# Kernel optimization log

Hardware: AMD Instinct MI355X
Metric: run time of the kernel (lower is better)

The kernel has to match this reference:

```python
import jax, jax.numpy as jnp
import numpy as np

N, NS, D, HID = 8192, 512, 1024, 1024  # nodes, num_edges, f_dim, mlp hidden (max(f_dim,128))


def layernorm(x, g, b, eps=1e-5):
    m = x.mean(-1, keepdims=True)
    v = x.var(-1, keepdims=True)
    return (x - m) / jnp.sqrt(v + eps) * g + b


def mask_topk(a, kk):
    # keep only the top-kk entries of each row (vectorized version of mask_attn)
    _, idx = jax.lax.top_k(a, kk)
    rows = jnp.arange(a.shape[0])[:, None]
    mask = jnp.zeros(a.shape, a.dtype).at[rows, idx].set(1.0)
    return a * mask


def setup_inputs() -> dict:
    key = jax.random.key(0)
    ks = jax.random.split(key, 16)
    xavier = lambda k, i, o: jax.random.uniform(k, (i, o), jnp.float32, -1.0, 1.0) * np.sqrt(6.0 / (i + o))
    return {
        "inputs": jax.random.normal(ks[0], (N, D), jnp.float32),
        "noise": jax.random.normal(ks[1], (NS, D), jnp.float32),
        "edges_mu": jax.random.normal(ks[2], (1, D), jnp.float32),
        "edges_logsigma": xavier(ks[3], 1, D),
        "Wq": xavier(ks[4], D, D), "bq": jnp.zeros((D,), jnp.float32),
        "Wk": xavier(ks[5], D, D), "bk": jnp.zeros((D,), jnp.float32),
        "Wv": xavier(ks[6], D, D), "bv": jnp.zeros((D,), jnp.float32),
        "W1": xavier(ks[7], 2 * D, HID), "b1": jnp.zeros((HID,), jnp.float32),
        "W2": xavier(ks[8], HID, D), "b2": jnp.zeros((D,), jnp.float32),
        "g_in": jnp.ones((D,), jnp.float32), "b_in": jnp.zeros((D,), jnp.float32),
        "g_e": jnp.ones((D,), jnp.float32), "b_e": jnp.zeros((D,), jnp.float32),
        "k_n": 64,
        "k_e": 8,
    }


def reference(inputs, noise, edges_mu, edges_logsigma, Wq, bq, Wk, bk, Wv, bv,
              W1, b1, W2, b2, g_in, b_in, g_e, b_e, k_n, k_e):
    n, d = inputs.shape
    scale = d ** -0.5
    eps = 1e-8
    x = layernorm(inputs, g_in, b_in)                       # norm_input
    k = jax.nn.relu(x @ Wk + bk)                            # [N, D]
    v = jax.nn.relu(x @ Wv + bv)                            # [N, D]
    edges = edges_mu + jnp.exp(edges_logsigma) * noise      # [NS, D]
    # single iteration (iters=1)
    edges = layernorm(edges, g_e, b_e)                      # norm_edgs
    q = jax.nn.relu(edges @ Wq + bq)                        # [NS, D]
    dots = jnp.einsum('ni,mi->nm', q, k) * scale            # [NS, N]
    attn = jax.nn.softmax(dots, axis=1) + eps
    attn = attn / attn.sum(axis=1, keepdims=True)
    attn = mask_topk(attn, k_n)
    updates = jnp.einsum('nm,md->nd', attn, v)              # [NS, D]
    edges = jnp.concatenate([edges, updates], axis=1)       # [NS, 2D]
    edges = jax.nn.relu(edges @ W1 + b1) @ W2 + b2          # mlp -> [NS, D]
    q2 = x @ Wq + bq                                        # no relu in source
    k2 = jax.nn.relu(edges @ Wk + bk)                       # [NS, D]
    dots_v = jnp.einsum('ni,mi->nm', q2, k2) * scale        # [N, NS]
    attn_v = jax.nn.softmax(dots_v, axis=1)
    H = mask_topk(attn_v, k_e)
    return edges, H, dots
```

## Files before the change

kernel.cpp:

```cpp
#include <hip/hip_runtime.h>
#include <stdint.h>
#include <stddef.h>

typedef unsigned short u16;
typedef uint32_t u32;
typedef __bf16 bf16x8 __attribute__((ext_vector_type(8)));
typedef float f32x4 __attribute__((ext_vector_type(4)));

#define DEV __device__ __forceinline__

#define GLD16(g, l) __builtin_amdgcn_global_load_lds( \
    (const __attribute__((address_space(1))) u32*)(g), \
    (__attribute__((address_space(3))) u32*)(l), 16, 0, 0)

DEV float bf2f(u16 u){ union{uint32_t i; float f;} c; c.i=(uint32_t)u<<16; return c.f; }
DEV u16 f2bf(float f){ union{float f; uint32_t i;} c; c.f=f; uint32_t x=c.i;
  uint32_t r = x + 0x7FFFu + ((x>>16)&1u); return (u16)(r>>16); }
DEV uint32_t fmap(float f){ union{float f; uint32_t u;} c; c.f=f;
  return (c.u & 0x80000000u) ? ~c.u : (c.u | 0x80000000u); }
DEV float funmap(uint32_t u){ union{uint32_t u; float f;} c;
  c.u = (u & 0x80000000u) ? (u & 0x7FFFFFFFu) : ~u; return c.f; }
DEV void split2(float x, u16& h, u16& l){ h = f2bf(x); l = f2bf(x - bf2f(h)); }

DEV void xcd_swizzle(int& bx, int& by){
  const int gx = gridDim.x, nwg = gx * gridDim.y;
  const int b  = blockIdx.x + gx*blockIdx.y;
  const int sb = (b & 7)*(nwg >> 3) + (b >> 3);
  bx = sb % gx; by = sb / gx;
}

DEV float bredsum(float v, float* buf, int tid){
  #pragma unroll
  for(int o=32;o;o>>=1) v += __shfl_down(v,o);
  __syncthreads();
  if((tid&63)==0) buf[tid>>6]=v;
  __syncthreads();
  return buf[0]+buf[1]+buf[2]+buf[3];
}
DEV float bredmax(float v, float* buf, int tid){
  #pragma unroll
  for(int o=32;o;o>>=1) v = fmaxf(v, __shfl_down(v,o));
  __syncthreads();
  if((tid&63)==0) buf[tid>>6]=v;
  __syncthreads();
  return fmaxf(fmaxf(buf[0],buf[1]),fmaxf(buf[2],buf[3]));
}
DEV int bredsumi(int v, int* buf, int tid){
  #pragma unroll
  for(int o=32;o;o>>=1) v += __shfl_down(v,o);
  __syncthreads();
  if((tid&63)==0) buf[tid>>6]=v;
  __syncthreads();
  return buf[0]+buf[1]+buf[2]+buf[3];
}

template<bool RELU, int SK>
__global__ __launch_bounds__(256)
void gemm1_64(const u16* __restrict__ A, int lda,
              const u16* __restrict__ Bt, int ldb,
              const float* __restrict__ bias, float scale,
              u16* __restrict__ outb, float* __restrict__ outf,
              float* __restrict__ part,
              int K, int ldc, int M)
{
  __shared__ __align__(16) u16 As[64*32];
  __shared__ __align__(16) u16 Bs[128*32];
  const int tid = threadIdx.x, lane = tid&63, wave = tid>>6;
  const int m0 = blockIdx.y*64, n0 = blockIdx.x*128;
  const int wm = (wave>>1)*32, wn = (wave&1)*64;
  const int ml = lane&15, quad = lane>>4;
  const int ks = K / SK;
  const int kbeg = blockIdx.z * ks;
  const u16* pa  = A  + (size_t)(m0+(tid>>2))*lda + kbeg + (tid&3)*8;
  const u16* pb0 = Bt + (size_t)(n0+(tid>>2))*ldb + kbeg + (tid&3)*8;
  const u16* pb1 = Bt + (size_t)(n0+64+(tid>>2))*ldb + kbeg + (tid&3)*8;

  f32x4 acc[2][4];
  #pragma unroll
  for(int i=0;i<2;i++)
    #pragma unroll
    for(int j=0;j<4;j++) acc[i][j] = (f32x4){0.f,0.f,0.f,0.f};

  uint4 ra=*(const uint4*)pa, rb0=*(const uint4*)pb0, rb1=*(const uint4*)pb1;
  for(int k0=0;k0<ks;k0+=32){
    __syncthreads();
    *(uint4*)&As[tid*8]       = ra;
    *(uint4*)&Bs[tid*8]       = rb0;
    *(uint4*)&Bs[(256+tid)*8] = rb1;
    __syncthreads();
    if(k0+32<ks){
      ra  = *(const uint4*)(pa +k0+32);
      rb0 = *(const uint4*)(pb0+k0+32);
      rb1 = *(const uint4*)(pb1+k0+32);
    }
    bf16x8 af[2], bf[4];
    #pragma unroll
    for(int mi=0;mi<2;mi++) af[mi] = *(const bf16x8*)&As[(wm+mi*16+ml)*32 + quad*8];
    #pragma unroll
    for(int ni=0;ni<4;ni++) bf[ni] = *(const bf16x8*)&Bs[(wn+ni*16+ml)*32 + quad*8];
    #pragma unroll
    for(int mi=0;mi<2;mi++)
      #pragma unroll
      for(int ni=0;ni<4;ni++)
        acc[mi][ni] = __builtin_amdgcn_mfma_f32_16x16x32_bf16(af[mi], bf[ni], acc[mi][ni], 0,0,0);
  }
  #pragma unroll
  for(int mi=0;mi<2;mi++){
    const int rbase = m0 + wm + mi*16 + quad*4;
    #pragma unroll
    for(int ni=0;ni<4;ni++){
      const int col = n0 + wn + ni*16 + ml;
      if(SK==1){
        const float bv = bias ? bias[col] : 0.f;
        #pragma unroll
        for(int r=0;r<4;r++){
          float v = acc[mi][ni][r]*scale + bv;
          if(RELU) v = fmaxf(v, 0.f);
          const size_t idx = (size_t)(rbase + r)*ldc + col;
          if(outb) outb[idx] = f2bf(v);
          if(outf) outf[idx] = v;
        }
      }else{
        #pragma unroll
        for(int r=0;r<4;r++)
          part[((size_t)blockIdx.z*M + rbase + r)*ldc + col] = acc[mi][ni][r];
      }
    }
  }
}

template<bool RELU>
__global__ __launch_bounds__(256)
void gemm1_128(const u16* __restrict__ A, int lda,
               const u16* __restrict__ Bt, int ldb,
               const float* __restrict__ bias, float scale,
               u16* __restrict__ outb, float* __restrict__ outf,
               int K, int ldc)
{
  __shared__ __align__(16) u16 As[128*32];
  __shared__ __align__(16) u16 Bs[128*32];
  const int tid = threadIdx.x, lane = tid&63, wave = tid>>6;
  int bxs, bys; xcd_swizzle(bxs, bys);
  const int m0 = bys*128, n0 = bxs*128;
  const int wm = (wave>>1)*64, wn = (wave&1)*64;
  const int ml = lane&15, quad = lane>>4;
  const u16* pa0 = A  + (size_t)(m0+(tid>>2))*lda    + (tid&3)*8;
  const u16* pa1 = A  + (size_t)(m0+64+(tid>>2))*lda + (tid&3)*8;
  const u16* pb0 = Bt + (size_t)(n0+(tid>>2))*ldb    + (tid&3)*8;
  const u16* pb1 = Bt + (size_t)(n0+64+(tid>>2))*ldb + (tid&3)*8;

  f32x4 acc[4][4];
  #pragma unroll
  for(int i=0;i<4;i++)
    #pragma unroll
    for(int j=0;j<4;j++) acc[i][j] = (f32x4){0.f,0.f,0.f,0.f};

  uint4 ra0=*(const uint4*)pa0, ra1=*(const uint4*)pa1;
  uint4 rb0=*(const uint4*)pb0, rb1=*(const uint4*)pb1;
  for(int k0=0;k0<K;k0+=32){
    __syncthreads();
    *(uint4*)&As[tid*8]       = ra0;
    *(uint4*)&As[(256+tid)*8] = ra1;
    *(uint4*)&Bs[tid*8]       = rb0;
    *(uint4*)&Bs[(256+tid)*8] = rb1;
    __syncthreads();
    if(k0+32<K){
      ra0 = *(const uint4*)(pa0+k0+32);
      ra1 = *(const uint4*)(pa1+k0+32);
      rb0 = *(const uint4*)(pb0+k0+32);
      rb1 = *(const uint4*)(pb1+k0+32);
    }
    bf16x8 af[4], bf[4];
    #pragma unroll
    for(int mi=0;mi<4;mi++) af[mi] = *(const bf16x8*)&As[(wm+mi*16+ml)*32 + quad*8];
    #pragma unroll
    for(int ni=0;ni<4;ni++) bf[ni] = *(const bf16x8*)&Bs[(wn+ni*16+ml)*32 + quad*8];
    #pragma unroll
    for(int mi=0;mi<4;mi++)
      #pragma unroll
      for(int ni=0;ni<4;ni++)
        acc[mi][ni] = __builtin_amdgcn_mfma_f32_16x16x32_bf16(af[mi], bf[ni], acc[mi][ni], 0,0,0);
  }
  #pragma unroll
  for(int mi=0;mi<4;mi++){
    const int rbase = m0 + wm + mi*16 + quad*4;
    #pragma unroll
    for(int ni=0;ni<4;ni++){
      const int col = n0 + wn + ni*16 + ml;
      const float bv = bias ? bias[col] : 0.f;
      #pragma unroll
      for(int r=0;r<4;r++){
        float v = acc[mi][ni][r]*scale + bv;
        if(RELU) v = fmaxf(v, 0.f);
        const size_t idx = (size_t)(rbase + r)*ldc + col;
        if(outb) outb[idx] = f2bf(v);
        if(outf) outf[idx] = v;
      }
    }
  }
}

__global__ __launch_bounds__(512)
void gemm_kv_256(const u16* __restrict__ A, int lda,
                 const u16* __restrict__ Bt, int ldb,
                 const float* __restrict__ bk, const float* __restrict__ bv,
                 u16* __restrict__ kb, u16* __restrict__ vb, int K)
{
  __shared__ __align__(16) u16 As[4][256*32];
  __shared__ __align__(16) u16 Bs[4][256*32];
  const int tid = threadIdx.x, lane = tid&63, wave = tid>>6;
  int bxs, bys; xcd_swizzle(bxs, bys);
  const int m0 = bys*256, n0 = bxs*256;
  const int wmw = (wave>>2)*128, wnw = (wave&3)*64;
  const int ml = lane&15, quad = lane>>4;
  const int r0 = tid>>2,        c0 = (tid&3)*8;
  const int r1 = (tid+512)>>2,  c1 = ((tid+512)&3)*8;
  const u16* pa0 = A  + (size_t)(m0+r0)*lda + c0;
  const u16* pa1 = A  + (size_t)(m0+r1)*lda + c1;
  const u16* pb0 = Bt + (size_t)(n0+r0)*ldb + c0;
  const u16* pb1 = Bt + (size_t)(n0+r1)*ldb + c1;
  const int d0 = r0*32 + c0, d1 = r1*32 + c1;

  f32x4 acc[8][4];
  #pragma unroll
  for(int i=0;i<8;i++)
    #pragma unroll
    for(int j=0;j<4;j++) acc[i][j] = (f32x4){0.f,0.f,0.f,0.f};

  #define KV_STAGE(t, s) do{                    \
    GLD16(pa0 + (t)*32, &As[s][d0]);            \
    GLD16(pa1 + (t)*32, &As[s][d1]);            \
    GLD16(pb0 + (t)*32, &Bs[s][d0]);            \
    GLD16(pb1 + (t)*32, &Bs[s][d1]); }while(0)

  KV_STAGE(0,0); KV_STAGE(1,1); KV_STAGE(2,2);
  const int NT = K >> 5;
  for(int t=0;t<NT;t++){
    if(t+3<NT) KV_STAGE(t+3, (t+3)&3);
    const int rem = NT-1-t;
    if(rem>=3)      asm volatile("s_waitcnt vmcnt(12)" ::: "memory");
    else if(rem==2) asm volatile("s_waitcnt vmcnt(8)"  ::: "memory");
    else if(rem==1) asm volatile("s_waitcnt vmcnt(4)"  ::: "memory");
    else            asm volatile("s_waitcnt vmcnt(0)"  ::: "memory");
    __builtin_amdgcn_s_barrier();
    const int s = t&3;
    bf16x8 af[8], bf[4];
    #pragma unroll
    for(int mi=0;mi<8;mi++) af[mi] = *(const bf16x8*)&As[s][(wmw+mi*16+ml)*32 + quad*8];
    #pragma unroll
    for(int ni=0;ni<4;ni++) bf[ni] = *(const bf16x8*)&Bs[s][(wnw+ni*16+ml)*32 + quad*8];
    #pragma unroll
    for(int mi=0;mi<8;mi++)
      #pragma unroll
      for(int ni=0;ni<4;ni++)
        acc[mi][ni] = __builtin_amdgcn_mfma_f32_16x16x32_bf16(af[mi], bf[ni], acc[mi][ni], 0,0,0);
    __builtin_amdgcn_s_barrier();
  }
  #undef KV_STAGE

  #pragma unroll
  for(int mi=0;mi<8;mi++){
    const int rbase = m0 + wmw + mi*16 + quad*4;
    #pragma unroll
    for(int ni=0;ni<4;ni++){
      const int col = n0 + wnw + ni*16 + ml;
      const bool isv = col >= 1024;
      const int c2 = col & 1023;
      const float bb = isv ? bv[c2] : bk[c2];
      u16* outp = isv ? vb : kb;
      #pragma unroll
      for(int r=0;r<4;r++){
        const float v = fmaxf(acc[mi][ni][r] + bb, 0.f);
        outp[(size_t)(rbase + r)*1024 + c2] = f2bf(v);
      }
    }
  }
}

template<bool RELU, int SK>
__global__ __launch_bounds__(256)
void gemm3_64(const u16* __restrict__ Ah, const u16* __restrict__ Al, int lda,
              const u16* __restrict__ Bh, const u16* __restrict__ Bl, int ldb,
              const float* __restrict__ bias, float scale,
              u16* __restrict__ outh, u16* __restrict__ outl,
              float* __restrict__ outf, float* __restrict__ part,
              int K, int ldc, int M)
{
  __shared__ __align__(16) u16 AsH[64*32];
  __shared__ __align__(16) u16 AsL[64*32];
  __shared__ __align__(16) u16 BsH[128*32];
  __shared__ __align__(16) u16 BsL[128*32];
  const int tid = threadIdx.x, lane = tid&63, wave = tid>>6;
  const int m0 = blockIdx.y*64, n0 = blockIdx.x*128;
  const int wm = (wave>>1)*32, wn = (wave&1)*64;
  const int ml = lane&15, quad = lane>>4;
  const int ks = K / SK;
  const int kbeg = blockIdx.z * ks;
  const size_t ao  = (size_t)(m0+(tid>>2))*lda + kbeg + (tid&3)*8;
  const size_t bo0 = (size_t)(n0+(tid>>2))*ldb + kbeg + (tid&3)*8;
  const size_t bo1 = (size_t)(n0+64+(tid>>2))*ldb + kbeg + (tid&3)*8;

  f32x4 acc[2][4];
  #pragma unroll
  for(int i=0;i<2;i++)
    #pragma unroll
    for(int j=0;j<4;j++) acc[i][j] = (f32x4){0.f,0.f,0.f,0.f};

  uint4 rah=*(const uint4*)(Ah+ao),  ral=*(const uint4*)(Al+ao);
  uint4 rbh0=*(const uint4*)(Bh+bo0), rbl0=*(const uint4*)(Bl+bo0);
  uint4 rbh1=*(const uint4*)(Bh+bo1), rbl1=*(const uint4*)(Bl+bo1);
  for(int k0=0;k0<ks;k0+=32){
    __syncthreads();
    *(uint4*)&AsH[tid*8]       = rah;
    *(uint4*)&AsL[tid*8]       = ral;
    *(uint4*)&BsH[tid*8]       = rbh0;
    *(uint4*)&BsL[tid*8]       = rbl0;
    *(uint4*)&BsH[(256+tid)*8] = rbh1;
    *(uint4*)&BsL[(256+tid)*8] = rbl1;
    __syncthreads();
    if(k0+32<ks){
      const int s = k0+32;
      rah =*(const uint4*)(Ah+ao +s); ral =*(const uint4*)(Al+ao +s);
      rbh0=*(const uint4*)(Bh+bo0+s); rbl0=*(const uint4*)(Bl+bo0+s);
      rbh1=*(const uint4*)(Bh+bo1+s); rbl1=*(const uint4*)(Bl+bo1+s);
    }
    bf16x8 afh[2], afl[2], bfh[4], bfl[4];
    #pragma unroll
    for(int mi=0;mi<2;mi++){
      const int o = (wm+mi*16+ml)*32 + quad*8;
      afh[mi] = *(const bf16x8*)&AsH[o];
      afl[mi] = *(const bf16x8*)&AsL[o];
    }
    #pragma unroll
    for(int ni=0;ni<4;ni++){
      const int o = (wn+ni*16+ml)*32 + quad*8;
      bfh[ni] = *(const bf16x8*)&BsH[o];
      bfl[ni] = *(const bf16x8*)&BsL[o];
    }
    #pragma unroll
    for(int mi=0;mi<2;mi++)
      #pragma unroll
      for(int ni=0;ni<4;ni++){
        acc[mi][ni] = __builtin_amdgcn_mfma_f32_16x16x32_bf16(afh[mi], bfh[ni], acc[mi][ni], 0,0,0);
        acc[mi][ni] = __builtin_amdgcn_mfma_f32_16x16x32_bf16(afh[mi], bfl[ni], acc[mi][ni], 0,0,0);
        acc[mi][ni] = __builtin_amdgcn_mfma_f32_16x16x32_bf16(afl[mi], bfh[ni], acc[mi][ni], 0,0,0);
      }
  }
  #pragma unroll
  for(int mi=0;mi<2;mi++){
    const int rbase = m0 + wm + mi*16 + quad*4;
    #pragma unroll
    for(int ni=0;ni<4;ni++){
      const int col = n0 + wn + ni*16 + ml;
      if(SK==1){
        const float bv = bias ? bias[col] : 0.f;
        #pragma unroll
        for(int r=0;r<4;r++){
          float v = acc[mi][ni][r]*scale + bv;
          if(RELU) v = fmaxf(v, 0.f);
          const size_t idx = (size_t)(rbase + r)*ldc + col;
          if(outh){ u16 h, l; split2(v, h, l); outh[idx] = h; outl[idx] = l; }
          if(outf) outf[idx] = v;
        }
      }else{
        #pragma unroll
        for(int r=0;r<4;r++)
          part[((size_t)blockIdx.z*M + rbase + r)*ldc + col] = acc[mi][ni][r];
      }
    }
  }
}

__global__ __launch_bounds__(256)
void gemm3_128(const u16* __restrict__ Ah, const u16* __restrict__ Al, int lda,
               const u16* __restrict__ Bh, const u16* __restrict__ Bl, int ldb,
               const float* __restrict__ bias, float scale,
               float* __restrict__ outf, int K, int ldc)
{
  __shared__ __align__(16) u16 AsH[128*32];
  __shared__ __align__(16) u16 AsL[128*32];
  __shared__ __align__(16) u16 BsH[128*32];
  __shared__ __align__(16) u16 BsL[128*32];
  const int tid = threadIdx.x, lane = tid&63, wave = tid>>6;
  int bxs, bys; xcd_swizzle(bxs, bys);
  const int m0 = bys*128, n0 = bxs*128;
  const int wm = (wave>>1)*64, wn = (wave&1)*64;
  const int ml = lane&15, quad = lane>>4;
  const size_t ao0 = (size_t)(m0+(tid>>2))*lda    + (tid&3)*8;
  const size_t ao1 = (size_t)(m0+64+(tid>>2))*lda + (tid&3)*8;
  const size_t bo0 = (size_t)(n0+(tid>>2))*ldb    + (tid&3)*8;
  const size_t bo1 = (size_t)(n0+64+(tid>>2))*ldb + (tid&3)*8;

  f32x4 acc[4][4];
  #pragma unroll
  for(int i=0;i<4;i++)
    #pragma unroll
    for(int j=0;j<4;j++) acc[i][j] = (f32x4){0.f,0.f,0.f,0.f};

  uint4 rah0=*(const uint4*)(Ah+ao0), ral0=*(const uint4*)(Al+ao0);
  uint4 rah1=*(const uint4*)(Ah+ao1), ral1=*(const uint4*)(Al+ao1);
  uint4 rbh0=*(const uint4*)(Bh+bo0), rbl0=*(const uint4*)(Bl+bo0);
  uint4 rbh1=*(const uint4*)(Bh+bo1), rbl1=*(const uint4*)(Bl+bo1);
  for(int k0=0;k0<K;k0+=32){
    __syncthreads();
    *(uint4*)&AsH[tid*8]       = rah0;
    *(uint4*)&AsH[(256+tid)*8] = rah1;
    *(uint4*)&AsL[tid*8]       = ral0;
    *(uint4*)&AsL[(256+tid)*8] = ral1;
    *(uint4*)&BsH[tid*8]       = rbh0;
    *(uint4*)&BsH[(256+tid)*8] = rbh1;
    *(uint4*)&BsL[tid*8]       = rbl0;
    *(uint4*)&BsL[(256+tid)*8] = rbl1;
    __syncthreads();
    if(k0+32<K){
      const int s = k0+32;
      rah0=*(const uint4*)(Ah+ao0+s); ral0=*(const uint4*)(Al+ao0+s);
      rah1=*(const uint4*)(Ah+ao1+s); ral1=*(const uint4*)(Al+ao1+s);
      rbh0=*(const uint4*)(Bh+bo0+s); rbl0=*(const uint4*)(Bl+bo0+s);
      rbh1=*(const uint4*)(Bh+bo1+s); rbl1=*(const uint4*)(Bl+bo1+s);
    }
    bf16x8 afh[4], afl[4], bfh[4], bfl[4];
    #pragma unroll
    for(int mi=0;mi<4;mi++){
      const int o = (wm+mi*16+ml)*32 + quad*8;
      afh[mi] = *(const bf16x8*)&AsH[o];
      afl[mi] = *(const bf16x8*)&AsL[o];
    }
    #pragma unroll
    for(int ni=0;ni<4;ni++){
      const int o = (wn+ni*16+ml)*32 + quad*8;
      bfh[ni] = *(const bf16x8*)&BsH[o];
      bfl[ni] = *(const bf16x8*)&BsL[o];
    }
    #pragma unroll
    for(int mi=0;mi<4;mi++)
      #pragma unroll
      for(int ni=0;ni<4;ni++){
        acc[mi][ni] = __builtin_amdgcn_mfma_f32_16x16x32_bf16(afh[mi], bfh[ni], acc[mi][ni], 0,0,0);
        acc[mi][ni] = __builtin_amdgcn_mfma_f32_16x16x32_bf16(afh[mi], bfl[ni], acc[mi][ni], 0,0,0);
        acc[mi][ni] = __builtin_amdgcn_mfma_f32_16x16x32_bf16(afl[mi], bfh[ni], acc[mi][ni], 0,0,0);
      }
  }
  #pragma unroll
  for(int mi=0;mi<4;mi++){
    const int rbase = m0 + wm + mi*16 + quad*4;
    #pragma unroll
    for(int ni=0;ni<4;ni++){
      const int col = n0 + wn + ni*16 + ml;
      const float bv = bias ? bias[col] : 0.f;
      #pragma unroll
      for(int r=0;r<4;r++){
        const float v = acc[mi][ni][r]*scale + bv;
        outf[(size_t)(rbase + r)*ldc + col] = v;
      }
    }
  }
}

template<bool RELU, int SK>
__global__ __launch_bounds__(256)
void reduce_epi(const float* __restrict__ part, const float* __restrict__ bias,
                float scale, u16* __restrict__ outh, u16* __restrict__ outl,
                u16* __restrict__ outb, float* __restrict__ outf,
                size_t MN, int N,
                const float* __restrict__ bqv, float* __restrict__ bvout)
{
  __shared__ float buf[4];
  const int tid = threadIdx.x;
  const size_t i = ((size_t)blockIdx.x*256 + tid)*4;
  float4 s = *(const float4*)(part + i);
  #pragma unroll
  for(int z=1; z<SK; z++){
    const float4 t = *(const float4*)(part + (size_t)z*MN + i);
    s.x += t.x; s.y += t.y; s.z += t.z; s.w += t.w;
  }
  const int col = (int)(i % (size_t)N);
  float4 bv = bias ? *(const float4*)(bias + col) : (float4){0.f,0.f,0.f,0.f};
  float v[4] = { s.x*scale + bv.x, s.y*scale + bv.y, s.z*scale + bv.z, s.w*scale + bv.w };
  if(RELU){
    #pragma unroll
    for(int j=0;j<4;j++) v[j] = fmaxf(v[j], 0.f);
  }
  if(outh){
    ushort4 h4, l4;
    split2(v[0], h4.x, l4.x); split2(v[1], h4.y, l4.y);
    split2(v[2], h4.z, l4.z); split2(v[3], h4.w, l4.w);
    *(ushort4*)(outh + i) = h4;
    *(ushort4*)(outl + i) = l4;
  }
  if(outb){
    ushort4 b4;
    b4.x=f2bf(v[0]); b4.y=f2bf(v[1]); b4.z=f2bf(v[2]); b4.w=f2bf(v[3]);
    *(ushort4*)(outb + i) = b4;
  }
  if(outf) *(float4*)(outf + i) = (float4){v[0],v[1],v[2],v[3]};
  if(bvout){
    const float4 q = *(const float4*)(bqv + col);
    float d = q.x*v[0] + q.y*v[1] + q.z*v[2] + q.w*v[3];
    d = bredsum(d, buf, tid);
    if(tid==0) bvout[blockIdx.x] = d * 0.03125f;
  }
}

DEV void dev_tsplit(const float* in, u16* oh, u16* ol, int R, int C,
                    int bx, int by, int tid, float (*tile)[33])
{
  const int tx = tid & 31, ty = tid >> 5;
  #pragma unroll
  for(int i=0;i<32;i+=8)
    tile[ty+i][tx] = in[(size_t)(by*32+ty+i)*C + bx*32 + tx];
  __syncthreads();
  #pragma unroll
  for(int i=0;i<32;i+=8){
    const float v = tile[tx][ty+i];
    u16 h, l; split2(v, h, l);
    const size_t o = (size_t)(bx*32+ty+i)*R + by*32 + tx;
    oh[o] = h; if(ol) ol[o] = l;
  }
}
__global__ __launch_bounds__(256)
void prep_weights(const float* __restrict__ Wk, const float* __restrict__ W1,
                  const float* __restrict__ W2, const float* __restrict__ Wv,
                  const float* __restrict__ Wq,
                  u16* __restrict__ WkvTh, u16* __restrict__ WkTl,
                  u16* __restrict__ W1Th,  u16* __restrict__ W1Tl,
                  u16* __restrict__ W2Th,  u16* __restrict__ W2Tl,
                  u16* __restrict__ WqTh,
                  u16* __restrict__ Wqh,   u16* __restrict__ Wql)
{
  __shared__ float tile[32][33];
  const int id = blockIdx.x, tid = threadIdx.x;
  if(id < 1024){
    dev_tsplit(Wk, WkvTh, WkTl, 1024, 1024, id&31, id>>5, tid, tile);
  }else if(id < 3072){
    const int l = id - 1024;
    dev_tsplit(W1, W1Th, W1Tl, 2048, 1024, l&31, l>>5, tid, tile);
  }else if(id < 4096){
    const int l = id - 3072;
    dev_tsplit(W2, W2Th, W2Tl, 1024, 1024, l&31, l>>5, tid, tile);
  }else if(id < 5120){
    const int l = id - 4096;
    dev_tsplit(Wv, WkvTh + 1024*1024, nullptr, 1024, 1024, l&31, l>>5, tid, tile);
  }else if(id < 6144){
    const int l = id - 5120;
    dev_tsplit(Wq, WqTh, nullptr, 1024, 1024, l&31, l>>5, tid, tile);
  }else{
    const int l = id - 6144;
    const int i = l*256 + tid;
    const float4 v = ((const float4*)Wq)[i];
    ushort4 h4, l4;
    split2(v.x, h4.x, l4.x); split2(v.y, h4.y, l4.y);
    split2(v.z, h4.z, l4.z); split2(v.w, h4.w, l4.w);
    ((ushort4*)Wqh)[i] = h4; ((ushort4*)Wql)[i] = l4;
  }
}

__global__ __launch_bounds__(256)
void ln_all(const float* __restrict__ in, const float* __restrict__ g,
            const float* __restrict__ bb, u16* __restrict__ outh,
            u16* __restrict__ outl,
            const float* __restrict__ noise, const float* __restrict__ mu,
            const float* __restrict__ lsig, const float* __restrict__ ge,
            const float* __restrict__ be, u16* __restrict__ cath,
            u16* __restrict__ catl)
{
  __shared__ float buf[4];
  const int tid = threadIdx.x;
  const bool edge = blockIdx.x >= 8192;
  const int row = edge ? (blockIdx.x - 8192) : blockIdx.x;
  float v0,v1,v2,v3;
  if(!edge){
    const float4 xv = ((const float4*)(in + (size_t)row*1024))[tid];
    v0=xv.x; v1=xv.y; v2=xv.z; v3=xv.w;
  }else{
    const float4 nv  = ((const float4*)(noise + (size_t)row*1024))[tid];
    const float4 muv = ((const float4*)mu)[tid];
    const float4 lsv = ((const float4*)lsig)[tid];
    v0 = muv.x + expf(lsv.x)*nv.x;
    v1 = muv.y + expf(lsv.y)*nv.y;
    v2 = muv.z + expf(lsv.z)*nv.z;
    v3 = muv.w + expf(lsv.w)*nv.w;
  }
  float s  = bredsum(v0+v1+v2+v3, buf, tid);
  float s2 = bredsum(v0*v0+v1*v1+v2*v2+v3*v3, buf, tid);
  const float mean = s * (1.f/1024.f);
  const float var  = s2 * (1.f/1024.f) - mean*mean;
  const float rs   = 1.f / sqrtf(var + 1e-5f);
  const float4 gv = ((const float4*)(edge?ge:g))[tid];
  const float4 bv = ((const float4*)(edge?be:bb))[tid];
  float o0 = (v0-mean)*rs*gv.x + bv.x;
  float o1 = (v1-mean)*rs*gv.y + bv.y;
  float o2 = (v2-mean)*rs*gv.z + bv.z;
  float o3 = (v3-mean)*rs*gv.w + bv.w;
  ushort4 oh, ol;
  split2(o0, oh.x, ol.x); split2(o1, oh.y, ol.y);
  split2(o2, oh.z, ol.z); split2(o3, oh.w, ol.w);
  u16* ph = edge ? cath : outh;
  u16* pl = edge ? catl : outl;
  const int ostride = edge ? 2048 : 1024;
  ((ushort4*)(ph + (size_t)row*ostride))[tid] = oh;
  ((ushort4*)(pl + (size_t)row*ostride))[tid] = ol;
}

#define SWZ(i) ((i) ^ (((((unsigned)(i))>>5)&7u)<<2))
__global__ __launch_bounds__(256)
void softmax_topk_a(const float* __restrict__ dots, const int* __restrict__ knp,
                    int* __restrict__ tidx, float* __restrict__ tw)
{
  const int NC = 8192;
  __shared__ __align__(16) uint32_t us[8192];
  __shared__ float fbuf[4];
  __shared__ int ibuf[4];
  __shared__ int scan[256];
  __shared__ uint32_t hist[256];
  __shared__ uint32_t bcast;
  __shared__ int slot_ctr;
  const int row = blockIdx.x, tid = threadIdx.x;
  const int lane = tid & 63, wave = tid >> 6;
  const float* x = dots + (size_t)row * NC;

  float mx = -3.4e38f;
  #pragma unroll
  for(int it=0; it<8; ++it){
    const int i = (tid + it*256)*4;
    const float4 f = *(const float4*)(x + i);
    mx = fmaxf(fmaxf(mx, fmaxf(f.x,f.y)), fmaxf(f.z,f.w));
    uint4 u; u.x=fmap(f.x); u.y=fmap(f.y); u.z=fmap(f.z); u.w=fmap(f.w);
    *(uint4*)&us[SWZ(i)] = u;
  }
  mx = bredmax(mx, fbuf, tid);

  float se = 0.f;
  #pragma unroll
  for(int it=0; it<8; ++it){
    const int i = (tid + it*256)*4;
    const uint4 u = *(const uint4*)&us[SWZ(i)];
    se += expf(funmap(u.x)-mx) + expf(funmap(u.y)-mx)
        + expf(funmap(u.z)-mx) + expf(funmap(u.w)-mx);
  }
  se = bredsum(se, fbuf, tid);
  const float T = 1.f + (float)NC * 1e-8f;

  const int k = knp[0];
  const int base = tid*32;

  uint32_t prefix = 0;
  int remaining = k;
  #pragma unroll
  for(int shift=24; shift>=0; shift-=8){
    hist[tid] = 0;
    __syncthreads();
    const uint32_t himask = (shift==24) ? 0u : (0xFFFFFFFFu << (shift+8));
    #pragma unroll
    for(int j=0;j<32;j+=4){
      const uint4 u4 = *(const uint4*)&us[SWZ(base+j)];
      const uint32_t uu[4] = {u4.x,u4.y,u4.z,u4.w};
      #pragma unroll
      for(int t=0;t<4;t++)
        if((uu[t] & himask) == prefix) atomicAdd(&hist[(uu[t]>>shift)&255u], 1u);
    }
    __syncthreads();
    if(wave==0){
      const uint32_t h0=hist[4*lane], h1=hist[4*lane+1],
                     h2=hist[4*lane+2], h3=hist[4*lane+3];
      const uint32_t s3=h3, s2=h2+s3, s1=h1+s2, s0=h0+s1;
      uint32_t tsum = s0;
      #pragma unroll
      for(int o=1;o<64;o<<=1){
        const uint32_t vv = __shfl_down(tsum, o);
        if(lane + o < 64) tsum += vv;
      }
      const uint32_t excl = tsum - s0;
      const uint32_t r = (uint32_t)remaining;
      int cand = -1; uint32_t gsel = 0;
      if     (s3+excl >= r){ cand = 4*lane+3; gsel = excl; }
      else if(s2+excl >= r){ cand = 4*lane+2; gsel = s3+excl; }
      else if(s1+excl >= r){ cand = 4*lane+1; gsel = s2+excl; }
      else if(s0+excl >= r){ cand = 4*lane+0; gsel = s1+excl; }
      int bestc = cand; uint32_t bestg = gsel;
      #pragma unroll
      for(int o=32;o;o>>=1){
        const int oc = __shfl_xor(bestc, o);
        const uint32_t og = __shfl_xor(bestg, o);
        if(oc > bestc){ bestc = oc; bestg = og; }
      }
      if(lane==0) bcast = (uint32_t)bestc;
      remaining -= (int)bestg;
    }
    __syncthreads();
    prefix |= bcast << shift;
  }
  const uint32_t uth = prefix;

  int gt = 0, eq = 0;
  #pragma unroll
  for(int j=0;j<32;j+=4){
    const uint4 u4 = *(const uint4*)&us[SWZ(base+j)];
    gt += (u4.x>uth)+(u4.y>uth)+(u4.z>uth)+(u4.w>uth);
    eq += (u4.x==uth)+(u4.y==uth)+(u4.z==uth)+(u4.w==uth);
  }
  const int c1 = bredsumi(gt, ibuf, tid);
  __syncthreads();
  scan[tid] = eq;
  __syncthreads();
  #pragma unroll
  for(int o=1;o<256;o<<=1){
    int t = (tid>=o) ? scan[tid-o] : 0;
    __syncthreads();
    scan[tid] += t;
    __syncthreads();
  }
  int eq_rank = scan[tid] - eq;
  const int budget = k - c1;
  if(tid==0) slot_ctr = 0;
  __syncthreads();
  #pragma unroll 2
  for(int j=0;j<32;j+=4){
    const uint4 u4 = *(const uint4*)&us[SWZ(base+j)];
    const uint32_t uu[4] = {u4.x,u4.y,u4.z,u4.w};
    #pragma unroll
    for(int t=0;t<4;t++){
      const uint32_t u = uu[t];
      bool sel = (u > uth);
      if(u == uth){ sel = (eq_rank < budget); eq_rank++; }
      if(sel){
        const int s = atomicAdd(&slot_ctr, 1);
        const float f = funmap(u);
        const float w = (expf(f - mx)/se + 1e-8f) / T;
        if(s < 128){ tidx[row*128 + s] = base + j + t; tw[row*128 + s] = w; }
      }
    }
  }
}

__global__ __launch_bounds__(256)
void gather_updates(const int* __restrict__ tidx, const float* __restrict__ tw,
                    const int* __restrict__ knp, const u16* __restrict__ v,
                    u16* __restrict__ cath, u16* __restrict__ catl)
{
  __shared__ int   idx_s[128];
  __shared__ float w_s[128];
  const int row = blockIdx.x, tid = threadIdx.x;
  const int kk = knp[0];
  if(tid < 128){
    idx_s[tid] = (tid < kk) ? (tidx[row*128+tid] & 8191) : 0;
    w_s[tid]   = (tid < kk) ? tw[row*128+tid] : 0.f;
  }
  __syncthreads();
  const int c = tid*4;
  float a0=0,a1=0,a2=0,a3=0;
  for(int j=0;j<kk && j<128;j++){
    const ushort4 vv = *(const ushort4*)&v[(size_t)idx_s[j]*1024 + c];
    const float w = w_s[j];
    a0 += w*bf2f(vv.x); a1 += w*bf2f(vv.y); a2 += w*bf2f(vv.z); a3 += w*bf2f(vv.w);
  }
  ushort4 oh, ol;
  split2(a0, oh.x, ol.x); split2(a1, oh.y, ol.y);
  split2(a2, oh.z, ol.z); split2(a3, oh.w, ol.w);
  ((ushort4*)(cath + (size_t)row*2048 + 1024))[tid] = oh;
  ((ushort4*)(catl + (size_t)row*2048 + 1024))[tid] = ol;
}

__global__ __launch_bounds__(256)
void softmax_topk_h_wave(const float* __restrict__ dv, const int* __restrict__ kep,
                         float* __restrict__ H)
{
  const int wave = threadIdx.x >> 6, lane = threadIdx.x & 63;
  const int row = blockIdx.x*4 + wave;
  const float* x = dv + (size_t)row*512 + lane*8;
  const float4 a = *(const float4*)x;
  const float4 b = *(const float4*)(x+4);
  float vals[8] = {a.x,a.y,a.z,a.w,b.x,b.y,b.z,b.w};

  float mx = vals[0];
  #pragma unroll
  for(int j=1;j<8;j++) mx = fmaxf(mx, vals[j]);
  #pragma unroll
  for(int o=32;o;o>>=1) mx = fmaxf(mx, __shfl_xor(mx, o));
  float e[8], se = 0.f;
  #pragma unroll
  for(int j=0;j<8;j++){ e[j] = expf(vals[j]-mx); se += e[j]; }
  #pragma unroll
  for(int o=32;o;o>>=1) se += __shfl_xor(se, o);
  const float inv = 1.f/se;

  const int k = kep[0];
  unsigned int selmask = 0;
  for(int r=0;r<k;r++){
    unsigned long long best = 0;
    #pragma unroll
    for(int j=0;j<8;j++){
      if(!((selmask>>j)&1u)){
        const unsigned long long key =
          ((unsigned long long)fmap(vals[j]) << 9) | (unsigned long long)(511 - (lane*8+j));
        if(key > best) best = key;
      }
    }
    #pragma unroll
    for(int o=32;o;o>>=1){
      const unsigned long long other = __shfl_xor(best, o);
      if(other > best) best = other;
    }
    const int bidx = 511 - (int)(best & 511ull);
    if((bidx>>3) == lane) selmask |= 1u << (bidx & 7);
  }

  float4 o0, o1;
  o0.x = (selmask&  1u) ? e[0]*inv : 0.f;
  o0.y = (selmask&  2u) ? e[1]*inv : 0.f;
  o0.z = (selmask&  4u) ? e[2]*inv : 0.f;
  o0.w = (selmask&  8u) ? e[3]*inv : 0.f;
  o1.x = (selmask& 16u) ? e[4]*inv : 0.f;
  o1.y = (selmask& 32u) ? e[5]*inv : 0.f;
  o1.z = (selmask& 64u) ? e[6]*inv : 0.f;
  o1.w = (selmask&128u) ? e[7]*inv : 0.f;
  float* outp = H + (size_t)row*512 + lane*8;
  *(float4*)outp     = o0;
  *(float4*)(outp+4) = o1;
}

extern "C" void kernel_launch(void* const* d_in, const int* in_sizes, int n_in,
                              void* d_out, int out_size, void* d_ws, size_t ws_size,
                              hipStream_t stream)
{
  const float* inputs = (const float*)d_in[0];
  const float* noise  = (const float*)d_in[1];
  const float* emu    = (const float*)d_in[2];
  const float* elsig  = (const float*)d_in[3];
  const float* Wq = (const float*)d_in[4];  const float* bq = (const float*)d_in[5];
  const float* Wk = (const float*)d_in[6];  const float* bk = (const float*)d_in[7];
  const float* Wv = (const float*)d_in[8];  const float* bv = (const float*)d_in[9];
  const float* W1 = (const float*)d_in[10]; const float* b1 = (const float*)d_in[11];
  const float* W2 = (const float*)d_in[12]; const float* b2 = (const float*)d_in[13];
  const float* g_in = (const float*)d_in[14]; const float* b_in = (const float*)d_in[15];
  const float* g_e  = (const float*)d_in[16]; const float* b_e  = (const float*)d_in[17];
  const int* knp = (const int*)d_in[18];
  const int* kep = (const int*)d_in[19];

  float* out = (float*)d_out;
  float* out_edges = out;
  float* out_H     = out + 512*1024;
  float* out_dots  = out + 512*1024 + 8192*512;

  char* p = (char*)d_ws;
  const size_t MB = 1024ull*1024;
  u16* xh = (u16*)(p + 0*MB);
  u16* xl = (u16*)(p + 16*MB);
  u16* kb = (u16*)(p + 32*MB);
  u16* vb = (u16*)(p + 48*MB);
  float* dotsvf = (float*)(p + 32*MB);
  u16* WkvTh = (u16*)(p + 64*MB);
  u16* WkTl  = (u16*)(p + 68*MB);
  u16* WqTh  = (u16*)(p + 70*MB);
  u16* Wqh   = (u16*)(p + 72*MB);  u16* Wql  = (u16*)(p + 74*MB);
  u16* W1Th  = (u16*)(p + 76*MB);  u16* W1Tl = (u16*)(p + 80*MB);
  u16* W2Th  = (u16*)(p + 84*MB);  u16* W2Tl = (u16*)(p + 86*MB);
  u16* cath = (u16*)(p + 88*MB);  u16* catl = (u16*)(p + 90*MB);
  u16* qmb  = (u16*)(p + 92*MB);
  u16* h1h  = (u16*)(p + 93*MB);  u16* h1l  = (u16*)(p + 94*MB);
  u16* eoh  = (u16*)(p + 95*MB);  u16* eol  = (u16*)(p + 96*MB);
  u16* k2h  = (u16*)(p + 97*MB);  u16* k2l  = (u16*)(p + 98*MB);
  u16* Gth  = (u16*)(p + 99*MB);  u16* Gtl  = (u16*)(p + 100*MB);
  int*   tidx  = (int*)  (p + 101*MB);
  float* tw    = (float*)(p + 101*MB + 256*1024);
  float* biasv = (float*)(p + 101*MB + 512*1024);
  float* part  = (float*)(p + 104*MB);


  prep_weights<<<7168,256,0,stream>>>(Wk, W1, W2, Wv, Wq,
                                      WkvTh, WkTl, W1Th, W1Tl, W2Th, W2Tl,
                                      WqTh, Wqh, Wql);
  ln_all<<<8704,256,0,stream>>>(inputs, g_in, b_in, xh, xl,
                                noise, emu, elsig, g_e, b_e, cath, catl);

  const size_t MN = 512ull*1024;
  gemm_kv_256<<<dim3(8,32),512,0,stream>>>(xh,1024, WkvTh,1024, bk, bv,
                                           kb, vb, 1024);
  gemm1_64<false,4><<<dim3(8,8,4),256,0,stream>>>(cath,2048, WqTh,1024, nullptr, 1.f,
                                                  nullptr,nullptr, part, 1024,1024,512);
  reduce_epi<true,4><<<512,256,0,stream>>>(part, bq, 1.f, nullptr,nullptr, qmb,nullptr,
                                           MN, 1024, nullptr, nullptr);
  gemm1_128<false><<<dim3(64,4),256,0,stream>>>(qmb,1024, kb,1024, nullptr, 0.03125f,
                                                nullptr,out_dots, 1024,8192);
  softmax_topk_a<<<512,256,0,stream>>>(out_dots, knp, tidx, tw);
  gather_updates<<<512,256,0,stream>>>(tidx, tw, knp, vb, cath, catl);

  gemm3_64<false,4><<<dim3(8,8,4),256,0,stream>>>(cath,catl,2048, W1Th,W1Tl,2048,
                                                  nullptr,1.f, nullptr,nullptr,nullptr,
                                                  part, 2048,1024,512);
  reduce_epi<true,4><<<512,256,0,stream>>>(part, b1, 1.f, h1h,h1l, nullptr,nullptr,
                                           MN, 1024, nullptr, nullptr);
  gemm3_64<false,4><<<dim3(8,8,4),256,0,stream>>>(h1h,h1l,1024, W2Th,W2Tl,1024,
                                                  nullptr,1.f, nullptr,nullptr,nullptr,
                                                  part, 1024,1024,512);
  reduce_epi<false,4><<<512,256,0,stream>>>(part, b2, 1.f, eoh,eol, nullptr,out_edges,
                                            MN, 1024, nullptr, nullptr);
  gemm3_64<false,4><<<dim3(8,8,4),256,0,stream>>>(eoh,eol,1024, WkvTh,WkTl,1024,
                                                  nullptr,1.f, nullptr,nullptr,nullptr,
                                                  part, 1024,1024,512);
  reduce_epi<true,4><<<512,256,0,stream>>>(part, bk, 1.f, k2h,k2l, nullptr,nullptr,
                                           MN, 1024, bq, biasv);
  gemm3_64<false,4><<<dim3(8,8,4),256,0,stream>>>(k2h,k2l,1024, Wqh,Wql,1024,
                                                  nullptr,1.f, nullptr,nullptr,nullptr,
                                                  part, 1024,1024,512);
  reduce_epi<false,4><<<512,256,0,stream>>>(part, nullptr, 1.f, Gth,Gtl, nullptr,nullptr,
                                            MN, 1024, nullptr, nullptr);
  gemm3_128<<<dim3(4,64),256,0,stream>>>(xh,xl,1024, Gth,Gtl,1024,
                                         biasv, 0.03125f, dotsvf, 1024,512);
  softmax_topk_h_wave<<<2048,256,0,stream>>>(dotsvf, kep, out_H);
}
```

Before: 378.7 us.

## Use 4-stage async global-to-LDS pipeline in gemm1_128 and gemm3_128

Replaces the register-staged double buffering in two GEMM kernels with a 4-deep ring of LDS buffers filled by direct global_load_lds instructions. Explicit vmcnt waits and barriers control when each stage may be consumed and overwritten. The aim is to hide global memory latency and skip the register round trip on the way to LDS. In exchange LDS use grows fourfold (128KB for gemm3), which lowers occupancy and may run into LDS capacity limits.

```diff
diff --git a/kernel.cpp b/kernel.cpp
--- a/kernel.cpp
+++ b/kernel.cpp
@@ -137,17 +137,19 @@
                u16* __restrict__ outb, float* __restrict__ outf,
                int K, int ldc)
 {
-  __shared__ __align__(16) u16 As[128*32];
-  __shared__ __align__(16) u16 Bs[128*32];
+  __shared__ __align__(16) u16 As[4][128*32];
+  __shared__ __align__(16) u16 Bs[4][128*32];
   const int tid = threadIdx.x, lane = tid&63, wave = tid>>6;
   int bxs, bys; xcd_swizzle(bxs, bys);
   const int m0 = bys*128, n0 = bxs*128;
   const int wm = (wave>>1)*64, wn = (wave&1)*64;
   const int ml = lane&15, quad = lane>>4;
-  const u16* pa0 = A  + (size_t)(m0+(tid>>2))*lda    + (tid&3)*8;
-  const u16* pa1 = A  + (size_t)(m0+64+(tid>>2))*lda + (tid&3)*8;
-  const u16* pb0 = Bt + (size_t)(n0+(tid>>2))*ldb    + (tid&3)*8;
-  const u16* pb1 = Bt + (size_t)(n0+64+(tid>>2))*ldb + (tid&3)*8;
+  const int r0 = tid>>2, c0 = (tid&3)*8;
+  const u16* pa0 = A  + (size_t)(m0+r0)*lda    + c0;
+  const u16* pa1 = A  + (size_t)(m0+64+r0)*lda + c0;
+  const u16* pb0 = Bt + (size_t)(n0+r0)*ldb    + c0;
+  const u16* pb1 = Bt + (size_t)(n0+64+r0)*ldb + c0;
+  const int d0 = r0*32 + c0, d1 = d0 + 64*32;
 
   f32x4 acc[4][4];
   #pragma unroll
@@ -155,32 +157,37 @@
     #pragma unroll
     for(int j=0;j<4;j++) acc[i][j] = (f32x4){0.f,0.f,0.f,0.f};
 
-  uint4 ra0=*(const uint4*)pa0, ra1=*(const uint4*)pa1;
-  uint4 rb0=*(const uint4*)pb0, rb1=*(const uint4*)pb1;
-  for(int k0=0;k0<K;k0+=32){
-    __syncthreads();
-    *(uint4*)&As[tid*8]       = ra0;
-    *(uint4*)&As[(256+tid)*8] = ra1;
-    *(uint4*)&Bs[tid*8]       = rb0;
-    *(uint4*)&Bs[(256+tid)*8] = rb1;
-    __syncthreads();
-    if(k0+32<K){
-      ra0 = *(const uint4*)(pa0+k0+32);
-      ra1 = *(const uint4*)(pa1+k0+32);
-      rb0 = *(const uint4*)(pb0+k0+32);
-      rb1 = *(const uint4*)(pb1+k0+32);
-    }
+  #define G1_STAGE(t, s) do{                \
+    GLD16(pa0 + (t)*32, &As[s][d0]);        \
+    GLD16(pa1 + (t)*32, &As[s][d1]);        \
+    GLD16(pb0 + (t)*32, &Bs[s][d0]);        \
+    GLD16(pb1 + (t)*32, &Bs[s][d1]); }while(0)
+
+  G1_STAGE(0,0); G1_STAGE(1,1); G1_STAGE(2,2);
+  const int NT = K >> 5;
+  for(int t=0;t<NT;t++){
+    if(t+3<NT) G1_STAGE(t+3, (t+3)&3);
+    const int rem = NT-1-t;
+    if(rem>=3)      asm volatile("s_waitcnt vmcnt(12)" ::: "memory");
+    else if(rem==2) asm volatile("s_waitcnt vmcnt(8)"  ::: "memory");
+    else if(rem==1) asm volatile("s_waitcnt vmcnt(4)"  ::: "memory");
+    else            asm volatile("s_waitcnt vmcnt(0)"  ::: "memory");
+    __builtin_amdgcn_s_barrier();
+    const int s = t&3;
     bf16x8 af[4], bf[4];
     #pragma unroll
-    for(int mi=0;mi<4;mi++) af[mi] = *(const bf16x8*)&As[(wm+mi*16+ml)*32 + quad*8];
-    #pragma unroll
-    for(int ni=0;ni<4;ni++) bf[ni] = *(const bf16x8*)&Bs[(wn+ni*16+ml)*32 + quad*8];
+    for(int mi=0;mi<4;mi++) af[mi] = *(const bf16x8*)&As[s][(wm+mi*16+ml)*32 + quad*8];
+    #pragma unroll
+    for(int ni=0;ni<4;ni++) bf[ni] = *(const bf16x8*)&Bs[s][(wn+ni*16+ml)*32 + quad*8];
     #pragma unroll
     for(int mi=0;mi<4;mi++)
       #pragma unroll
       for(int ni=0;ni<4;ni++)
         acc[mi][ni] = __builtin_amdgcn_mfma_f32_16x16x32_bf16(af[mi], bf[ni], acc[mi][ni], 0,0,0);
-  }
+    __builtin_amdgcn_s_barrier();
+  }
+  #undef G1_STAGE
+
   #pragma unroll
   for(int mi=0;mi<4;mi++){
     const int rbase = m0 + wm + mi*16 + quad*4;
@@ -377,19 +384,25 @@
                const float* __restrict__ bias, float scale,
                float* __restrict__ outf, int K, int ldc)
 {
-  __shared__ __align__(16) u16 AsH[128*32];
-  __shared__ __align__(16) u16 AsL[128*32];
-  __shared__ __align__(16) u16 BsH[128*32];
-  __shared__ __align__(16) u16 BsL[128*32];
+  __shared__ __align__(16) u16 AsH[4][128*32];
+  __shared__ __align__(16) u16 AsL[4][128*32];
+  __shared__ __align__(16) u16 BsH[4][128*32];
+  __shared__ __align__(16) u16 BsL[4][128*32];
   const int tid = threadIdx.x, lane = tid&63, wave = tid>>6;
   int bxs, bys; xcd_swizzle(bxs, bys);
   const int m0 = bys*128, n0 = bxs*128;
   const int wm = (wave>>1)*64, wn = (wave&1)*64;
   const int ml = lane&15, quad = lane>>4;
-  const size_t ao0 = (size_t)(m0+(tid>>2))*lda    + (tid&3)*8;
-  const size_t ao1 = (size_t)(m0+64+(tid>>2))*lda + (tid&3)*8;
-  const size_t bo0 = (size_t)(n0+(tid>>2))*ldb    + (tid&3)*8;
-  const size_t bo1 = (size_t)(n0+64+(tid>>2))*ldb + (tid&3)*8;
+  const int r0 = tid>>2, c0 = (tid&3)*8;
+  const u16* pah0 = Ah + (size_t)(m0+r0)*lda    + c0;
+  const u16* pah1 = Ah + (size_t)(m0+64+r0)*lda + c0;
+  const u16* pal0 = Al + (size_t)(m0+r0)*lda    + c0;
+  const u16* pal1 = Al + (size_t)(m0+64+r0)*lda + c0;
+  const u16* pbh0 = Bh + (size_t)(n0+r0)*ldb    + c0;
+  const u16* pbh1 = Bh + (size_t)(n0+64+r0)*ldb + c0;
+  const u16* pbl0 = Bl + (size_t)(n0+r0)*ldb    + c0;
+  const u16* pbl1 = Bl + (size_t)(n0+64+r0)*ldb + c0;
+  const int d0 = r0*32 + c0, d1 = d0 + 64*32;
 
   f32x4 acc[4][4];
   #pragma unroll
@@ -397,40 +410,39 @@
     #pragma unroll
     for(int j=0;j<4;j++) acc[i][j] = (f32x4){0.f,0.f,0.f,0.f};
 
-  uint4 rah0=*(const uint4*)(Ah+ao0), ral0=*(const uint4*)(Al+ao0);
-  uint4 rah1=*(const uint4*)(Ah+ao1), ral1=*(const uint4*)(Al+ao1);
-  uint4 rbh0=*(const uint4*)(Bh+bo0), rbl0=*(const uint4*)(Bl+bo0);
-  uint4 rbh1=*(const uint4*)(Bh+bo1), rbl1=*(const uint4*)(Bl+bo1);
-  for(int k0=0;k0<K;k0+=32){
-    __syncthreads();
-    *(uint4*)&AsH[tid*8]       = rah0;
-    *(uint4*)&AsH[(256+tid)*8] = rah1;
-    *(uint4*)&AsL[tid*8]       = ral0;
-    *(uint4*)&AsL[(256+tid)*8] = ral1;
-    *(uint4*)&BsH[tid*8]       = rbh0;
-    *(uint4*)&BsH[(256+tid)*8] = rbh1;
-    *(uint4*)&BsL[tid*8]       = rbl0;
-    *(uint4*)&BsL[(256+tid)*8] = rbl1;
-    __syncthreads();
-    if(k0+32<K){
-      const int s = k0+32;
-      rah0=*(const uint4*)(Ah+ao0+s); ral0=*(const uint4*)(Al+ao0+s);
-      rah1=*(const uint4*)(Ah+ao1+s); ral1=*(const uint4*)(Al+ao1+s);
-      rbh0=*(const uint4*)(Bh+bo0+s); rbl0=*(const uint4*)(Bl+bo0+s);
-      rbh1=*(const uint4*)(Bh+bo1+s); rbl1=*(const uint4*)(Bl+bo1+s);
-    }
+  #define G3_STAGE(t, s) do{                 \
+    GLD16(pah0 + (t)*32, &AsH[s][d0]);       \
+    GLD16(pah1 + (t)*32, &AsH[s][d1]);       \
+    GLD16(pal0 + (t)*32, &AsL[s][d0]);       \
+    GLD16(pal1 + (t)*32, &AsL[s][d1]);       \
+    GLD16(pbh0 + (t)*32, &BsH[s][d0]);       \
+    GLD16(pbh1 + (t)*32, &BsH[s][d1]);       \
+    GLD16(pbl0 + (t)*32, &BsL[s][d0]);       \
+    GLD16(pbl1 + (t)*32, &BsL[s][d1]); }while(0)
+
+  G3_STAGE(0,0); G3_STAGE(1,1); G3_STAGE(2,2);
+  const int NT = K >> 5;
+  for(int t=0;t<NT;t++){
+    if(t+3<NT) G3_STAGE(t+3, (t+3)&3);
+    const int rem = NT-1-t;
+    if(rem>=3)      asm volatile("s_waitcnt vmcnt(24)" ::: "memory");
+    else if(rem==2) asm volatile("s_waitcnt vmcnt(16)" ::: "memory");
+    else if(rem==1) asm volatile("s_waitcnt vmcnt(8)"  ::: "memory");
+    else            asm volatile("s_waitcnt vmcnt(0)"  ::: "memory");
+    __builtin_amdgcn_s_barrier();
+    const int s = t&3;
     bf16x8 afh[4], afl[4], bfh[4], bfl[4];
     #pragma unroll
     for(int mi=0;mi<4;mi++){
       const int o = (wm+mi*16+ml)*32 + quad*8;
-      afh[mi] = *(const bf16x8*)&AsH[o];
-      afl[mi] = *(const bf16x8*)&AsL[o];
+      afh[mi] = *(const bf16x8*)&AsH[s][o];
+      afl[mi] = *(const bf16x8*)&AsL[s][o];
     }
     #pragma unroll
     for(int ni=0;ni<4;ni++){
       const int o = (wn+ni*16+ml)*32 + quad*8;
-      bfh[ni] = *(const bf16x8*)&BsH[o];
-      bfl[ni] = *(const bf16x8*)&BsL[o];
+      bfh[ni] = *(const bf16x8*)&BsH[s][o];
+      bfl[ni] = *(const bf16x8*)&BsL[s][o];
     }
     #pragma unroll
     for(int mi=0;mi<4;mi++)
@@ -440,7 +452,10 @@
         acc[mi][ni] = __builtin_amdgcn_mfma_f32_16x16x32_bf16(afh[mi], bfl[ni], acc[mi][ni], 0,0,0);
         acc[mi][ni] = __builtin_amdgcn_mfma_f32_16x16x32_bf16(afl[mi], bfh[ni], acc[mi][ni], 0,0,0);
       }
-  }
+    __builtin_amdgcn_s_barrier();
+  }
+  #undef G3_STAGE
+
   #pragma unroll
   for(int mi=0;mi<4;mi++){
     const int rbase = m0 + wm + mi*16 + quad*4;
@@ -866,7 +881,6 @@
   float* biasv = (float*)(p + 101*MB + 512*1024);
   float* part  = (float*)(p + 104*MB);
 
-
   prep_weights<<<7168,256,0,stream>>>(Wk, W1, W2, Wv, Wq,
                                       WkvTh, WkTl, W1Th, W1Tl, W2Th, W2Tl,
                                       WqTh, Wqh, Wql);
```

Result: slower. 392.5 us (+3.6%).
